# Kernel tuning notes

Hardware: AMD Instinct MI355X
Metric: run time of the kernel (lower is better)

Reference implementation:

```python
import jax, jax.numpy as jnp
import numpy as np

N_NODES = 200_000
N_EVENTS = 50_000
MEM = 128
RAW = 64
TD = 64
HEADS = 2
DH = MEM // HEADS
EDGE_DIM = RAW + TD
MSG_IN = 2 * MEM + RAW + TD


def _time_enc(x, w, b):
    # PyG TimeEncoder: cos(Linear(t)) with Linear(1, time_dim)
    return jnp.cos(x[..., None] * w + b)


def setup_inputs() -> dict:
    key = jax.random.key(0)
    ks = jax.random.split(key, 30)

    def w(i, shape, scale=None):
        s = scale if scale is not None else 1.0 / np.sqrt(shape[-1])
        return jax.random.normal(ks[i], shape, jnp.float32) * s

    src = jax.random.randint(ks[0], (N_EVENTS,), 0, N_NODES)
    dst = jax.random.randint(ks[1], (N_EVENTS,), 0, N_NODES)
    t = jnp.sort(jax.random.uniform(ks[2], (N_EVENTS,), jnp.float32, 0.0, 1e4))
    return dict(
        memory=w(3, (N_NODES, MEM), 1.0),
        last_update=jnp.zeros((N_NODES,), jnp.float32),
        t=t,
        msg=w(4, (N_EVENTS, RAW), 1.0),
        src=src, dst=dst,
        time_w=w(5, (TD,), 1.0), time_b=w(6, (TD,), 1.0),
        gru_Wih=w(7, (3 * MEM, MSG_IN)), gru_bih=w(8, (3 * MEM,), 0.02),
        gru_Whh=w(9, (3 * MEM, MEM)), gru_bhh=w(10, (3 * MEM,), 0.02),
        Wq=w(11, (MEM, MEM)), bq=w(12, (MEM,), 0.02),
        Wk=w(13, (MEM, MEM)), bk=w(14, (MEM,), 0.02),
        Wv=w(15, (MEM, MEM)), bv=w(16, (MEM,), 0.02),
        We=w(17, (MEM, EDGE_DIM)),
        Wskip=w(18, (MEM, MEM)), bskip=w(19, (MEM,), 0.02),
        Wls=w(20, (MEM, MEM)), bls=w(21, (MEM,), 0.02),
        Wld=w(22, (MEM, MEM)), bld=w(23, (MEM,), 0.02),
        Wlf=w(24, (1, MEM)), blf=w(25, (1,), 0.02),
    )


def reference(memory, last_update, t, msg, src, dst, time_w, time_b,
              gru_Wih, gru_bih, gru_Whh, gru_bhh,
              Wq, bq, Wk, bk, Wv, bv, We, Wskip, bskip,
              Wls, bls, Wld, bld, Wlf, blf):
    N, D = memory.shape
    E = src.shape[0]
    # --- 1. IdentityMessage: raw store for src side and dst side of each event ---
    dt_s = t - last_update[src]
    dt_d = t - last_update[dst]
    m_s = jnp.concatenate([memory[src], memory[dst], msg, _time_enc(dt_s, time_w, time_b)], -1)
    m_d = jnp.concatenate([memory[dst], memory[src], msg, _time_enc(dt_d, time_w, time_b)], -1)
    all_msg = jnp.concatenate([m_s, m_d], 0)        # [2E, MSG_IN]
    all_id = jnp.concatenate([src, dst], 0)         # [2E]
    all_t = jnp.concatenate([t, t], 0)              # [2E]
    # --- 2. LastAggregator: keep the latest message per target node ---
    pos = jnp.arange(2 * E, dtype=jnp.int32)
    last_pos = jnp.full((N,), -1, jnp.int32).at[all_id].max(pos)
    is_last = last_pos[all_id] == pos               # [2E], exactly one True per touched node
    # --- 3. GRUCell memory update (computed per message, scattered for the last one) ---
    h = memory[all_id]
    gi = all_msg @ gru_Wih.T + gru_bih
    gh = h @ gru_Whh.T + gru_bhh
    ir, iz, i_n = jnp.split(gi, 3, -1)
    hr, hz, h_n = jnp.split(gh, 3, -1)
    r = jax.nn.sigmoid(ir + hr)
    zg = jax.nn.sigmoid(iz + hz)
    n = jnp.tanh(i_n + r * h_n)
    h_new = (1.0 - zg) * n + zg * h
    memory_new = memory.at[all_id].add(jnp.where(is_last[:, None], h_new - h, 0.0))
    last_update_new = last_update.at[all_id].max(jnp.where(is_last, all_t, -jnp.inf))
    # --- 4. GraphAttentionEmbedding: TransformerConv(heads=2, edge_dim) in eval mode ---
    rel_t = last_update_new[src] - t
    edge_attr = jnp.concatenate([_time_enc(rel_t, time_w, time_b), msg], -1)  # [E, EDGE_DIM]
    e_proj = edge_attr @ We.T                                                  # [E, MEM]
    q = (memory_new @ Wq.T + bq).reshape(N, HEADS, DH)
    k = (memory_new[src] @ Wk.T + bk + e_proj).reshape(E, HEADS, DH)
    v = (memory_new[src] @ Wv.T + bv + e_proj).reshape(E, HEADS, DH)
    logit = jnp.einsum('ehd,ehd->eh', q[dst], k) / np.sqrt(DH).astype(np.float32)
    mx = jnp.full((N, HEADS), -jnp.inf, memory.dtype).at[dst].max(logit)
    a = jnp.exp(logit - mx[dst])
    denom = jax.ops.segment_sum(a, dst, num_segments=N)
    attn = a / denom[dst]                                                      # segment softmax over incoming edges
    out = jnp.zeros((N, HEADS, DH), memory.dtype).at[dst].add(attn[..., None] * v)
    z = out.reshape(N, D) + memory_new @ Wskip.T + bskip                       # root/skip connection
    # --- 5. LinkPredictor on event endpoints ---
    hlp = jax.nn.relu(z[src] @ Wls.T + bls + z[dst] @ Wld.T + bld)
    return hlp @ Wlf.T + blf                                                   # [E, 1]
```

## Files before the change

kernel.cpp:

```cpp
#include <hip/hip_runtime.h>
#include <math.h>

#define NN 200000
#define NE 50000
#define D 128

#define WGRU_SZ  196608
#define WATTN_SZ 147456
#define WSKP_SZ  16384
#define WLINK_SZ 32768

__device__ __forceinline__ float frcp_(float x) { return __builtin_amdgcn_rcpf(x); }
__device__ __forceinline__ float fsig_(float x) { return frcp_(1.f + __expf(-x)); }
__device__ __forceinline__ float ftanh_(float x) {
    float xc = fminf(fmaxf(x, -15.f), 15.f);
    float t = __expf(2.f * xc);
    return (t - 1.f) * frcp_(t + 1.f);
}

__device__ __forceinline__ unsigned short f2bf(float f) {
    unsigned int u = __float_as_uint(f);
    u = (u + 0x7fffu + ((u >> 16) & 1u)) >> 16;
    return (unsigned short)u;
}
__device__ __forceinline__ float bf2f(unsigned short b) {
    return __uint_as_float(((unsigned int)b) << 16);
}

typedef short bf16x8 __attribute__((ext_vector_type(8)));
typedef float f32x4  __attribute__((ext_vector_type(4)));

__global__ void k_initprep(const float* __restrict__ Wih, const float* __restrict__ Whh,
                           const float* __restrict__ Wk, const float* __restrict__ Wv,
                           const float* __restrict__ Wq, const float* __restrict__ We,
                           const float* __restrict__ Wskip,
                           const float* __restrict__ Wls, const float* __restrict__ Wld,
                           const int* __restrict__ src, const int* __restrict__ dst,
                           unsigned short* __restrict__ wgru,
                           unsigned short* __restrict__ wattn,
                           unsigned short* __restrict__ wskp,
                           unsigned short* __restrict__ wlink,
                           int* __restrict__ last_pos, int* __restrict__ count) {
    int idx = blockIdx.x * 256 + threadIdx.x;
    if (idx == 0) *count = 0;
    if (idx < 2 * NE) {
        int id = (idx < NE) ? src[idx] : dst[idx - NE];
        atomicMax(&last_pos[id], idx + 1);
    }
    if (idx >= 49152 + 36864 + 4096 + 8192) return;
    float4 v;
    unsigned short* dstp;
    int ncopies, stride;
    if (idx < 49152) {
        int n = idx / 96;
        int c = (idx - n * 96) * 4;
        if (n < 384) {
            v = *(const float4*)&Wih[n * 384 + c];
            if (n < 256 && c < 128) {
                const float4 w2 = *(const float4*)&Whh[n * 128 + c];
                v.x += w2.x; v.y += w2.y; v.z += w2.z; v.w += w2.w;
            }
        } else {
            if (c >= 128) return;
            v = *(const float4*)&Whh[(n - 128) * 128 + c];
        }
        dstp = &wgru[n * 384 + c]; ncopies = 8; stride = WGRU_SZ;
    } else if (idx < 49152 + 36864) {
        int i2 = idx - 49152;
        int n = i2 / 96;
        int c = (i2 - n * 96) * 4;
        if (n < 256) {
            const float* Wm = (n < 128) ? Wk : Wv;
            int nn = n & 127;
            if (c < 128)       v = *(const float4*)&Wm[nn * 128 + c];
            else if (c < 256)  v = *(const float4*)&We[nn * 128 + (c - 128)];
            else return;
        } else {
            if (c < 256) return;
            v = *(const float4*)&Wq[(n - 256) * 128 + (c - 256)];
        }
        dstp = &wattn[n * 384 + c]; ncopies = 4; stride = WATTN_SZ;
    } else if (idx < 49152 + 36864 + 4096) {
        int i3 = idx - 49152 - 36864;
        int n = i3 / 32;
        int c = (i3 - n * 32) * 4;
        v = *(const float4*)&Wskip[n * 128 + c];
        dstp = &wskp[n * 128 + c]; ncopies = 8; stride = WSKP_SZ;
    } else {
        int i4 = idx - 49152 - 36864 - 4096;
        int n = i4 / 64;
        int c = (i4 - n * 64) * 4;
        if (c < 128) v = *(const float4*)&Wls[n * 128 + c];
        else         v = *(const float4*)&Wld[n * 128 + (c - 128)];
        dstp = &wlink[n * 256 + c]; ncopies = 4; stride = WLINK_SZ;
    }
    ushort4 b;
    b.x = f2bf(v.x); b.y = f2bf(v.y); b.z = f2bf(v.z); b.w = f2bf(v.w);
    for (int r = 0; r < ncopies; ++r)
        *(ushort4*)(dstp + (size_t)r * stride) = b;
}

__global__ void k_compact(const int* __restrict__ src, const int* __restrict__ dst,
                          const int* __restrict__ last_pos,
                          int* __restrict__ count, int* __restrict__ clist,
                          int* __restrict__ node2slot, int* __restrict__ head) {
    int i = blockIdx.x * blockDim.x + threadIdx.x;
    if (i < 2 * NE) {
        int id = (i < NE) ? src[i] : dst[i - NE];
        if (last_pos[id] == i + 1) {
            int s = atomicAdd(count, 1);
            clist[s] = i;
            node2slot[id] = s;
            head[s] = -1;
        }
    }
}

#define GMB 64
__global__ __launch_bounds__(512) void k_gru(
    const float* __restrict__ memp, const float* __restrict__ lup,
    const float* __restrict__ tp, const float* __restrict__ msgp,
    const int* __restrict__ srcp, const int* __restrict__ dstp,
    const float* __restrict__ twp, const float* __restrict__ tbp,
    const int* __restrict__ clist,
    const unsigned short* __restrict__ wgru_all,
    const float* __restrict__ bih, const float* __restrict__ bhh,
    const unsigned short* __restrict__ wskp_all, const float* __restrict__ bskip,
    const int* __restrict__ countp,
    unsigned short* __restrict__ mem_new, unsigned short* __restrict__ zbf,
    float* __restrict__ lu_new)
{
    __shared__ alignas(16) unsigned short Xs[64][392];
    __shared__ int sid[64], sother[64], se[64];
    __shared__ float sdt[64];
    int cnt = *countp;
    int base = blockIdx.x * GMB;
    if (base >= cnt) return;
    int tid = threadIdx.x;
    const unsigned short* __restrict__ wgru = wgru_all + (size_t)(blockIdx.x & 7) * WGRU_SZ;
    const unsigned short* __restrict__ wskp = wskp_all + (size_t)(blockIdx.x & 7) * WSKP_SZ;

    if (tid < 64) {
        int ii = base + tid;
        bool valid = ii < cnt;
        int iw = clist[valid ? ii : (cnt - 1)];
        int e = (iw < NE) ? iw : (iw - NE);
        int id    = (iw < NE) ? srcp[e] : dstp[e];
        int oth   = (iw < NE) ? dstp[e] : srcp[e];
        sid[tid] = id; sother[tid] = oth; se[tid] = e;
        float tt = tp[e];
        float lu = lup[id];
        sdt[tid] = tt - lu;
        if (valid) lu_new[id] = fmaxf(lu, tt);
    }
    __syncthreads();
    {
        int m = tid >> 3, li = tid & 7;
        int id = sid[m], oth = sother[m], e = se[m];
        float dt = sdt[m];
        #pragma unroll
        for (int j = 0; j < 12; ++j) {
            int c4 = li + 8 * j;
            float4 v;
            if (c4 < 32)      v = *(const float4*)&memp[id * D + c4 * 4];
            else if (c4 < 64) v = *(const float4*)&memp[oth * D + (c4 - 32) * 4];
            else if (c4 < 80) v = *(const float4*)&msgp[e * 64 + (c4 - 64) * 4];
            else {
                int c0 = (c4 - 80) * 4;
                v.x = cosf(dt * twp[c0 + 0] + tbp[c0 + 0]);
                v.y = cosf(dt * twp[c0 + 1] + tbp[c0 + 1]);
                v.z = cosf(dt * twp[c0 + 2] + tbp[c0 + 2]);
                v.w = cosf(dt * twp[c0 + 3] + tbp[c0 + 3]);
            }
            ushort4 b;
            b.x = f2bf(v.x); b.y = f2bf(v.y); b.z = f2bf(v.z); b.w = f2bf(v.w);
            *(ushort4*)&Xs[m][c4 * 4] = b;
        }
    }
    __syncthreads();

    int lane = tid & 63, w = tid >> 6;
    int q = lane >> 4, l15 = lane & 15;
    int q8 = q * 8, w16 = w * 16;

    f32x4 acc[4][4];
    #pragma unroll
    for (int mt = 0; mt < 4; ++mt)
        #pragma unroll
        for (int g = 0; g < 4; ++g)
            acc[mt][g] = (f32x4)(0.0f);

#define GRU_STEP(NG)                                                                      \
    {                                                                                     \
        bf16x8 a[4];                                                                      \
        _Pragma("unroll")                                                                 \
        for (int mt = 0; mt < 4; ++mt) a[mt] = *(const bf16x8*)&Xs[mt * 16 + l15][k0 + q8]; \
        _Pragma("unroll")                                                                 \
        for (int g = 0; g < NG; ++g) {                                                    \
            const bf16x8 b = *(const bf16x8*)&wgru[(g * 128 + w16 + l15) * 384 + k0 + q8]; \
            _Pragma("unroll")                                                             \
            for (int mt = 0; mt < 4; ++mt)                                                \
                acc[mt][g] = __builtin_amdgcn_mfma_f32_16x16x32_bf16(a[mt], b, acc[mt][g], 0, 0, 0); \
        }                                                                                 \
    }

    #pragma unroll 2
    for (int ks = 0; ks < 4; ++ks) { int k0 = ks * 32; GRU_STEP(4) }
    #pragma unroll 2
    for (int ks = 4; ks < 12; ++ks) { int k0 = ks * 32; GRU_STEP(3) }
#undef GRU_STEP

    float nval[4][4];
    {
        int c = w16 + l15;
        float br  = bih[c]       + bhh[c];
        float bz  = bih[128 + c] + bhh[128 + c];
        float bin = bih[256 + c];
        float bhn = bhh[256 + c];
        #pragma unroll
        for (int mt = 0; mt < 4; ++mt) {
            #pragma unroll
            for (int reg = 0; reg < 4; ++reg) {
                int m = mt * 16 + q * 4 + reg;
                float r  = fsig_(acc[mt][0][reg] + br);
                float zg = fsig_(acc[mt][1][reg] + bz);
                float n  = ftanh_(acc[mt][2][reg] + bin + r * (acc[mt][3][reg] + bhn));
                float hv = bf2f(Xs[m][c]);
                nval[mt][reg] = (1.f - zg) * n + zg * hv;
            }
        }
    }

    __syncthreads();
    {
        int c = w16 + l15;
        #pragma unroll
        for (int mt = 0; mt < 4; ++mt)
            #pragma unroll
            for (int reg = 0; reg < 4; ++reg)
                Xs[mt * 16 + q * 4 + reg][c] = f2bf(nval[mt][reg]);
    }
    __syncthreads();

    {
        #pragma unroll
        for (int j = 0; j < 2; ++j) {
            int ch = tid + 512 * j;
            int m = ch >> 4, c8 = ch & 15;
            *(uint4*)&mem_new[(size_t)(base + m) * D + c8 * 8] = *(const uint4*)&Xs[m][c8 * 8];
        }
    }

    f32x4 acc2[4];
    #pragma unroll
    for (int mt = 0; mt < 4; ++mt) acc2[mt] = (f32x4)(0.0f);
    #pragma unroll
    for (int ks = 0; ks < 4; ++ks) {
        int k0 = ks * 32;
        bf16x8 a[4];
        #pragma unroll
        for (int mt = 0; mt < 4; ++mt) a[mt] = *(const bf16x8*)&Xs[mt * 16 + l15][k0 + q8];
        const bf16x8 b = *(const bf16x8*)&wskp[(w16 + l15) * 128 + k0 + q8];
        #pragma unroll
        for (int mt = 0; mt < 4; ++mt)
            acc2[mt] = __builtin_amdgcn_mfma_f32_16x16x32_bf16(a[mt], b, acc2[mt], 0, 0, 0);
    }
    __syncthreads();
    {
        int ch = w16 + l15;
        float b = bskip[ch];
        #pragma unroll
        for (int mt = 0; mt < 4; ++mt)
            #pragma unroll
            for (int reg = 0; reg < 4; ++reg)
                Xs[mt * 16 + q * 4 + reg][ch] = f2bf(acc2[mt][reg] + b);
    }
    __syncthreads();
    {
        #pragma unroll
        for (int j = 0; j < 2; ++j) {
            int ch = tid + 512 * j;
            int m = ch >> 4, c8 = ch & 15;
            *(uint4*)&zbf[(size_t)(base + m) * D + c8 * 8] = *(const uint4*)&Xs[m][c8 * 8];
        }
    }
}

#define AMB 32
__global__ __launch_bounds__(256) void k_attnA(
    const int* __restrict__ srcp, const int* __restrict__ dstp,
    const float* __restrict__ tp, const float* __restrict__ msgp,
    const float* __restrict__ twp, const float* __restrict__ tbp,
    const float* __restrict__ lu_new, const int* __restrict__ node2slot,
    const unsigned short* __restrict__ mem_new,
    const unsigned short* __restrict__ wattn_all,
    const float* __restrict__ bq, const float* __restrict__ bk, const float* __restrict__ bv,
    unsigned short* __restrict__ vbuf, float* __restrict__ abuf,
    int* __restrict__ head, int* __restrict__ next)
{
    __shared__ alignas(16) unsigned short Xs[32][392];
    unsigned short (*kLb)[136] = (unsigned short(*)[136])(&Xs[0][0]);
    unsigned short (*qLb)[136] = (unsigned short(*)[136])(&Xs[0][0] + 4352);
    __shared__ float sa[AMB][2];
    __shared__ int sslot[AMB], sdslot[AMB];
    __shared__ float srel[AMB];
    int tid = threadIdx.x;
    int e0 = blockIdx.x * AMB;
    const unsigned short* __restrict__ wattn = wattn_all + (size_t)(blockIdx.x & 3) * WATTN_SZ;
    {
        int gid = blockIdx.x * 256 + tid;
        if (gid < NE) {
            int sl = node2slot[dstp[gid]];
            next[gid] = atomicExch(&head[sl], gid);
        }
    }
    if (tid < AMB) {
        int e = e0 + tid; if (e >= NE) e = NE - 1;
        int s = srcp[e], dd = dstp[e];
        sslot[tid]  = node2slot[s];
        sdslot[tid] = node2slot[dd];
        srel[tid] = lu_new[s] - tp[e];
    }
    __syncthreads();
    {
        int m = tid >> 3, li = tid & 7;
        int e = e0 + m; if (e >= NE) e = NE - 1;
        int ssl = sslot[m], dsl = sdslot[m];
        float rel = srel[m];
        uint4* xrow = (uint4*)&Xs[m][0];
        const uint4* srow = (const uint4*)&mem_new[(size_t)ssl * D];
        const uint4* drow = (const uint4*)&mem_new[(size_t)dsl * D];
        #pragma unroll
        for (int j = 0; j < 2; ++j) {
            xrow[li + 8 * j]      = srow[li + 8 * j];
            xrow[32 + li + 8 * j] = drow[li + 8 * j];
        }
        {
            int c0 = li * 8;
            ushort4 lo, hi;
            lo.x = f2bf(cosf(rel * twp[c0 + 0] + tbp[c0 + 0]));
            lo.y = f2bf(cosf(rel * twp[c0 + 1] + tbp[c0 + 1]));
            lo.z = f2bf(cosf(rel * twp[c0 + 2] + tbp[c0 + 2]));
            lo.w = f2bf(cosf(rel * twp[c0 + 3] + tbp[c0 + 3]));
            hi.x = f2bf(cosf(rel * twp[c0 + 4] + tbp[c0 + 4]));
            hi.y = f2bf(cosf(rel * twp[c0 + 5] + tbp[c0 + 5]));
            hi.z = f2bf(cosf(rel * twp[c0 + 6] + tbp[c0 + 6]));
            hi.w = f2bf(cosf(rel * twp[c0 + 7] + tbp[c0 + 7]));
            *(ushort4*)&Xs[m][128 + c0]     = lo;
            *(ushort4*)&Xs[m][128 + c0 + 4] = hi;
        }
        {
            float4 a = *(const float4*)&msgp[e * 64 + li * 8];
            float4 b = *(const float4*)&msgp[e * 64 + li * 8 + 4];
            ushort4 lo, hi;
            lo.x = f2bf(a.x); lo.y = f2bf(a.y); lo.z = f2bf(a.z); lo.w = f2bf(a.w);
            hi.x = f2bf(b.x); hi.y = f2bf(b.y); hi.z = f2bf(b.z); hi.w = f2bf(b.w);
            *(ushort4*)&Xs[m][192 + li * 8]     = lo;
            *(ushort4*)&Xs[m][192 + li * 8 + 4] = hi;
        }
    }
    __syncthreads();

    int lane = tid & 63, w = tid >> 6;
    int q = lane >> 4, l15 = lane & 15;
    int q8 = q * 8;

    f32x4 acc[2][6];
    #pragma unroll
    for (int mt = 0; mt < 2; ++mt)
        #pragma unroll
        for (int jj = 0; jj < 6; ++jj) acc[mt][jj] = (f32x4)(0.0f);

    #pragma unroll 2
    for (int ks = 0; ks < 8; ++ks) {
        int k0 = ks * 32;
        const bf16x8 a0 = *(const bf16x8*)&Xs[l15][k0 + q8];
        const bf16x8 a1 = *(const bf16x8*)&Xs[16 + l15][k0 + q8];
        #pragma unroll
        for (int jj = 0; jj < 4; ++jj) {
            int nt = w + 4 * jj;
            const bf16x8 b = *(const bf16x8*)&wattn[(nt * 16 + l15) * 384 + k0 + q8];
            acc[0][jj] = __builtin_amdgcn_mfma_f32_16x16x32_bf16(a0, b, acc[0][jj], 0, 0, 0);
            acc[1][jj] = __builtin_amdgcn_mfma_f32_16x16x32_bf16(a1, b, acc[1][jj], 0, 0, 0);
        }
    }
    #pragma unroll 2
    for (int ks = 8; ks < 12; ++ks) {
        int k0 = ks * 32;
        const bf16x8 a0 = *(const bf16x8*)&Xs[l15][k0 + q8];
        const bf16x8 a1 = *(const bf16x8*)&Xs[16 + l15][k0 + q8];
        #pragma unroll
        for (int jj = 4; jj < 6; ++jj) {
            int nt = w + 4 * jj;
            const bf16x8 b = *(const bf16x8*)&wattn[(nt * 16 + l15) * 384 + k0 + q8];
            acc[0][jj] = __builtin_amdgcn_mfma_f32_16x16x32_bf16(a0, b, acc[0][jj], 0, 0, 0);
            acc[1][jj] = __builtin_amdgcn_mfma_f32_16x16x32_bf16(a1, b, acc[1][jj], 0, 0, 0);
        }
    }

    __syncthreads();

    float vreg[2][2][4];
    #pragma unroll
    for (int jj = 0; jj < 6; ++jj) {
        int nt = w + 4 * jj;
        int gate = nt >> 3;
        int ch = (nt & 7) * 16 + l15;
        float bias = (gate == 0) ? bk[ch] : (gate == 1) ? bv[ch] : bq[ch];
        #pragma unroll
        for (int mt = 0; mt < 2; ++mt)
            #pragma unroll
            for (int reg = 0; reg < 4; ++reg) {
                int m = mt * 16 + q * 4 + reg;
                float val = acc[mt][jj][reg] + bias;
                if (gate == 0)      kLb[m][ch] = f2bf(val);
                else if (gate == 2) qLb[m][ch] = f2bf(val);
                else                vreg[jj - 2][mt][reg] = val;
            }
    }
    __syncthreads();
    #pragma unroll
    for (int pr = 0; pr < 16; ++pr) {
        int p2 = pr * 4 + w;
        int m = p2 >> 1, h = p2 & 1;
        float prod = bf2f(qLb[m][h * 64 + lane]) * bf2f(kLb[m][h * 64 + lane]);
        #pragma unroll
        for (int off = 32; off; off >>= 1) prod += __shfl_down(prod, off);
        if (lane == 0) {
            float a = __expf(prod * 0.125f);
            sa[m][h] = a;
            if (e0 + m < NE) abuf[(e0 + m) * 2 + h] = a;
        }
    }
    __syncthreads();
    {
        unsigned short (*vL)[136] = qLb;
        #pragma unroll
        for (int jv = 0; jv < 2; ++jv) {
            int ch = w * 16 + jv * 64 + l15;
            int h = jv;
            #pragma unroll
            for (int mt = 0; mt < 2; ++mt)
                #pragma unroll
                for (int reg = 0; reg < 4; ++reg) {
                    int m = mt * 16 + q * 4 + reg;
                    vL[m][ch] = f2bf(sa[m][h] * vreg[jv][mt][reg]);
                }
        }
        __syncthreads();
        #pragma unroll
        for (int j = 0; j < 2; ++j) {
            int chunk = tid + 256 * j;
            int row = chunk >> 4, c8 = chunk & 15;
            if (e0 + row < NE)
                *(uint4*)&vbuf[(size_t)(e0 + row) * D + c8 * 8] = *(const uint4*)&vL[row][c8 * 8];
        }
    }
}

__global__ __launch_bounds__(256) void k_gather(
    const int* __restrict__ countp, const int* __restrict__ head,
    const int* __restrict__ next, const float* __restrict__ abuf,
    const unsigned short* __restrict__ vbuf, unsigned short* __restrict__ zbf)
{
    int cnt = *countp;
    int slot = blockIdx.x * 32 + (threadIdx.x >> 3);
    if (slot >= cnt) return;
    int li = threadIdx.x & 7;
    int c0 = li * 16;
    int h = li >> 2;
    float vsum[16];
    #pragma unroll
    for (int j = 0; j < 16; ++j) vsum[j] = 0.f;
    float asum = 0.f;
    for (int e = head[slot]; e != -1; e = next[e]) {
        asum += abuf[e * 2 + h];
        uint4 v0 = *(const uint4*)&vbuf[(size_t)e * D + c0];
        uint4 v1 = *(const uint4*)&vbuf[(size_t)e * D + c0 + 8];
        const unsigned short* pv0 = (const unsigned short*)&v0;
        const unsigned short* pv1 = (const unsigned short*)&v1;
        #pragma unroll
        for (int j = 0; j < 8; ++j) { vsum[j] += bf2f(pv0[j]); vsum[8 + j] += bf2f(pv1[j]); }
    }
    if (asum > 0.f) {
        float rr = frcp_(asum);
        uint4 z0 = *(const uint4*)&zbf[(size_t)slot * D + c0];
        uint4 z1 = *(const uint4*)&zbf[(size_t)slot * D + c0 + 8];
        const unsigned short* pz0 = (const unsigned short*)&z0;
        const unsigned short* pz1 = (const unsigned short*)&z1;
        unsigned short o[16];
        #pragma unroll
        for (int j = 0; j < 8; ++j) {
            o[j]     = f2bf(bf2f(pz0[j]) + vsum[j] * rr);
            o[8 + j] = f2bf(bf2f(pz1[j]) + vsum[8 + j] * rr);
        }
        *(uint4*)&zbf[(size_t)slot * D + c0]     = *(const uint4*)&o[0];
        *(uint4*)&zbf[(size_t)slot * D + c0 + 8] = *(const uint4*)&o[8];
    }
}

__global__ __launch_bounds__(256) void k_link(
    const int* __restrict__ srcp, const int* __restrict__ dstp,
    const int* __restrict__ node2slot,
    const unsigned short* __restrict__ zbf,
    const unsigned short* __restrict__ wlink_all,
    const float* __restrict__ bls, const float* __restrict__ bld,
    const float* __restrict__ Wlf, const float* __restrict__ blf,
    float* __restrict__ outp)
{
    __shared__ alignas(16) unsigned short Xs[32][264];
    __shared__ int ssl[32], sdl[32];
    __shared__ float sred[32][4];
    int tid = threadIdx.x;
    int e0 = blockIdx.x * 32;
    const unsigned short* __restrict__ wlink = wlink_all + (size_t)(blockIdx.x & 3) * WLINK_SZ;
    if (tid < 32) {
        int e = e0 + tid; if (e >= NE) e = NE - 1;
        ssl[tid] = node2slot[srcp[e]];
        sdl[tid] = node2slot[dstp[e]];
    }
    __syncthreads();
    {
        int m = tid >> 3, li = tid & 7;
        uint4* xrow = (uint4*)&Xs[m][0];
        const uint4* srow = (const uint4*)&zbf[(size_t)ssl[m] * D];
        const uint4* drow = (const uint4*)&zbf[(size_t)sdl[m] * D];
        xrow[li]      = srow[li];
        xrow[li + 8]  = srow[li + 8];
        xrow[16 + li] = drow[li];
        xrow[24 + li] = drow[li + 8];
    }
    __syncthreads();

    int lane = tid & 63, w = tid >> 6;
    int q = lane >> 4, l15 = lane & 15;
    int q8 = q * 8;

    f32x4 acc[2][2];
    #pragma unroll
    for (int mt = 0; mt < 2; ++mt)
        #pragma unroll
        for (int jj = 0; jj < 2; ++jj) acc[mt][jj] = (f32x4)(0.0f);

    #pragma unroll
    for (int ks = 0; ks < 8; ++ks) {
        int k0 = ks * 32;
        const bf16x8 a0 = *(const bf16x8*)&Xs[l15][k0 + q8];
        const bf16x8 a1 = *(const bf16x8*)&Xs[16 + l15][k0 + q8];
        #pragma unroll
        for (int jj = 0; jj < 2; ++jj) {
            int nt = w + 4 * jj;
            const bf16x8 b = *(const bf16x8*)&wlink[(nt * 16 + l15) * 256 + k0 + q8];
            acc[0][jj] = __builtin_amdgcn_mfma_f32_16x16x32_bf16(a0, b, acc[0][jj], 0, 0, 0);
            acc[1][jj] = __builtin_amdgcn_mfma_f32_16x16x32_bf16(a1, b, acc[1][jj], 0, 0, 0);
        }
    }

    float p[2][4];
    #pragma unroll
    for (int mt = 0; mt < 2; ++mt)
        #pragma unroll
        for (int reg = 0; reg < 4; ++reg) p[mt][reg] = 0.f;
    #pragma unroll
    for (int jj = 0; jj < 2; ++jj) {
        int ch = (w + 4 * jj) * 16 + l15;
        float bias = bls[ch] + bld[ch];
        float wl = Wlf[ch];
        #pragma unroll
        for (int mt = 0; mt < 2; ++mt)
            #pragma unroll
            for (int reg = 0; reg < 4; ++reg)
                p[mt][reg] += fmaxf(acc[mt][jj][reg] + bias, 0.f) * wl;
    }
    #pragma unroll
    for (int mask = 1; mask < 16; mask <<= 1) {
        #pragma unroll
        for (int mt = 0; mt < 2; ++mt)
            #pragma unroll
            for (int reg = 0; reg < 4; ++reg)
                p[mt][reg] += __shfl_xor(p[mt][reg], mask);
    }
    if (l15 == 0) {
        #pragma unroll
        for (int mt = 0; mt < 2; ++mt)
            #pragma unroll
            for (int reg = 0; reg < 4; ++reg)
                sred[mt * 16 + q * 4 + reg][w] = p[mt][reg];
    }
    __syncthreads();
    if (tid < 32) {
        int e = e0 + tid;
        if (e < NE)
            outp[e] = sred[tid][0] + sred[tid][1] + sred[tid][2] + sred[tid][3] + blf[0];
    }
}

extern "C" void kernel_launch(void* const* d_in, const int* in_sizes, int n_in,
                              void* d_out, int out_size, void* d_ws, size_t ws_size,
                              hipStream_t stream)
{
    const float* memory      = (const float*)d_in[0];
    const float* last_update = (const float*)d_in[1];
    const float* t           = (const float*)d_in[2];
    const float* msg         = (const float*)d_in[3];
    const int*   src         = (const int*)d_in[4];
    const int*   dst         = (const int*)d_in[5];
    const float* time_w      = (const float*)d_in[6];
    const float* time_b      = (const float*)d_in[7];
    const float* gru_Wih     = (const float*)d_in[8];
    const float* gru_bih     = (const float*)d_in[9];
    const float* gru_Whh     = (const float*)d_in[10];
    const float* gru_bhh     = (const float*)d_in[11];
    const float* Wq          = (const float*)d_in[12];
    const float* bq          = (const float*)d_in[13];
    const float* Wk          = (const float*)d_in[14];
    const float* bk          = (const float*)d_in[15];
    const float* Wv          = (const float*)d_in[16];
    const float* bv          = (const float*)d_in[17];
    const float* We          = (const float*)d_in[18];
    const float* Wskip       = (const float*)d_in[19];
    const float* bskip       = (const float*)d_in[20];
    const float* Wls         = (const float*)d_in[21];
    const float* bls         = (const float*)d_in[22];
    const float* Wld         = (const float*)d_in[23];
    const float* bld         = (const float*)d_in[24];
    const float* Wlf         = (const float*)d_in[25];
    const float* blf         = (const float*)d_in[26];
    float* outp = (float*)d_out;

    char* ws = (char*)d_ws;
    int*   last_pos  = (int*)  (ws + 0);
    int*   node2slot = (int*)  (ws + 800000);
    float* lu_new    = (float*)(ws + 1600000);
    int*   count     = (int*)  (ws + 2400000);
    int*   clist     = (int*)  (ws + 2400016);
    unsigned short* wgru    = (unsigned short*)(ws + 79624592);
    unsigned short* wattn   = (unsigned short*)(ws + 82770320);
    unsigned short* wskp    = (unsigned short*)(ws + 83949968);
    unsigned short* wlink   = (unsigned short*)(ws + 84212112);
    unsigned short* mem_new = (unsigned short*)(ws + 84474256);
    unsigned short* zbf     = (unsigned short*)(ws + 110082448);
    unsigned short* vbuf    = (unsigned short*)(ws + 135690640);
    float* abuf = (float*)(ws + 148490640);
    int*   head = (int*)  (ws + 148890640);
    int*   next = (int*)  (ws + 149290768);

    k_initprep<<<(2 * NE + 255) / 256, 256, 0, stream>>>(
                 gru_Wih, gru_Whh, Wk, Wv, Wq, We, Wskip, Wls, Wld, src, dst,
                 wgru, wattn, wskp, wlink, last_pos, count);
    k_compact <<<(2 * NE + 255) / 256, 256, 0, stream>>>(src, dst, last_pos, count,
                 clist, node2slot, head);
    k_gru     <<<(2 * NE + GMB - 1) / GMB, 512, 0, stream>>>(memory, last_update, t, msg,
                 src, dst, time_w, time_b, clist, wgru, gru_bih, gru_bhh,
                 wskp, bskip, count, mem_new, zbf, lu_new);
    k_attnA   <<<(NE + AMB - 1) / AMB, 256, 0, stream>>>(src, dst, t, msg, time_w, time_b,
                 lu_new, node2slot, mem_new, wattn, bq, bk, bv, vbuf, abuf, head, next);
    k_gather  <<<(2 * NE + 31) / 32, 256, 0, stream>>>(count, head, next, abuf, vbuf, zbf);
    k_link    <<<(NE + 31) / 32, 256, 0, stream>>>(src, dst, node2slot, zbf,
                 wlink, bls, bld, Wlf, blf, outp);
}
```

Measured before the change: 385.3 us.

## Fold skip projection into link predictor weights via concatenated z rows

Removes the per-node skip GEMM from the GRU kernel by precomputing Wls·Wskip and Wld·Wskip (and the folded biases) at init. The GRU writes memory_new into the upper half of a 256-wide zcat row, and the gather kernel writes the attention output into the lower half. The link kernel then does a single K=512 GEMM over both halves, with 64 events per block. This trades a smaller GRU kernel and one fewer round trip through global memory for a larger link GEMM, a serial 128-length dot-product loop per thread at init, and an occupancy hint on k_gru.

Result: slower. 400.9 us (+4.0%).

```diff
diff --git a/kernel.cpp b/kernel.cpp
--- a/kernel.cpp
+++ b/kernel.cpp
@@ -4,11 +4,11 @@
 #define NN 200000
 #define NE 50000
 #define D 128
+#define ZROW 256
 
 #define WGRU_SZ  196608
 #define WATTN_SZ 147456
-#define WSKP_SZ  16384
-#define WLINK_SZ 32768
+#define WLNK2_SZ 65536
 
 __device__ __forceinline__ float frcp_(float x) { return __builtin_amdgcn_rcpf(x); }
 __device__ __forceinline__ float fsig_(float x) { return frcp_(1.f + __expf(-x)); }
@@ -33,13 +33,14 @@
 __global__ void k_initprep(const float* __restrict__ Wih, const float* __restrict__ Whh,
                            const float* __restrict__ Wk, const float* __restrict__ Wv,
                            const float* __restrict__ Wq, const float* __restrict__ We,
-                           const float* __restrict__ Wskip,
+                           const float* __restrict__ Wskip, const float* __restrict__ bskip,
                            const float* __restrict__ Wls, const float* __restrict__ Wld,
+                           const float* __restrict__ bls, const float* __restrict__ bld,
                            const int* __restrict__ src, const int* __restrict__ dst,
                            unsigned short* __restrict__ wgru,
                            unsigned short* __restrict__ wattn,
-                           unsigned short* __restrict__ wskp,
-                           unsigned short* __restrict__ wlink,
+                           unsigned short* __restrict__ wlink2,
+                           float* __restrict__ blink,
                            int* __restrict__ last_pos, int* __restrict__ count) {
     int idx = blockIdx.x * 256 + threadIdx.x;
     if (idx == 0) *count = 0;
@@ -47,7 +48,7 @@
         int id = (idx < NE) ? src[idx] : dst[idx - NE];
         atomicMax(&last_pos[id], idx + 1);
     }
-    if (idx >= 49152 + 36864 + 4096 + 8192) return;
+    if (idx >= 102528) return;
     float4 v;
     unsigned short* dstp;
     int ncopies, stride;
@@ -80,19 +81,39 @@
             v = *(const float4*)&Wq[(n - 256) * 128 + (c - 256)];
         }
         dstp = &wattn[n * 384 + c]; ncopies = 4; stride = WATTN_SZ;
-    } else if (idx < 49152 + 36864 + 4096) {
-        int i3 = idx - 49152 - 36864;
-        int n = i3 / 32;
-        int c = (i3 - n * 32) * 4;
-        v = *(const float4*)&Wskip[n * 128 + c];
-        dstp = &wskp[n * 128 + c]; ncopies = 8; stride = WSKP_SZ;
+    } else if (idx < 86016 + 8192) {
+        int i4 = idx - 86016;
+        int n = i4 >> 6;
+        int c = (i4 & 63) * 4;
+        int dc;
+        if (c < 128) { v = *(const float4*)&Wls[n * 128 + c];        dc = c; }
+        else         { v = *(const float4*)&Wld[n * 128 + (c - 128)]; dc = c + 128; }
+        dstp = &wlink2[n * 512 + dc]; ncopies = 4; stride = WLNK2_SZ;
+    } else if (idx < 94208 + 8192) {
+        int i5 = idx - 94208;
+        int n = i5 >> 6;
+        int g = i5 & 63;
+        const float* Wrow = (g < 32) ? &Wls[n * 128] : &Wld[n * 128];
+        int c = (g & 31) * 4;
+        float ax = 0.f, ay = 0.f, az = 0.f, aw = 0.f;
+        for (int j = 0; j < 128; ++j) {
+            float a = Wrow[j];
+            const float4 ws = *(const float4*)&Wskip[j * 128 + c];
+            ax += a * ws.x; ay += a * ws.y; az += a * ws.z; aw += a * ws.w;
+        }
+        ushort4 b4;
+        b4.x = f2bf(ax); b4.y = f2bf(ay); b4.z = f2bf(az); b4.w = f2bf(aw);
+        unsigned short* dp = &wlink2[n * 512 + ((g < 32) ? 128 : 384) + c];
+        for (int r = 0; r < 4; ++r)
+            *(ushort4*)(dp + (size_t)r * WLNK2_SZ) = b4;
+        return;
     } else {
-        int i4 = idx - 49152 - 36864 - 4096;
-        int n = i4 / 64;
-        int c = (i4 - n * 64) * 4;
-        if (c < 128) v = *(const float4*)&Wls[n * 128 + c];
-        else         v = *(const float4*)&Wld[n * 128 + (c - 128)];
-        dstp = &wlink[n * 256 + c]; ncopies = 4; stride = WLINK_SZ;
+        int n = idx - 102400;
+        float s = bls[n] + bld[n];
+        for (int j = 0; j < 128; ++j)
+            s += (Wls[n * 128 + j] + Wld[n * 128 + j]) * bskip[j];
+        blink[n] = s;
+        return;
     }
     ushort4 b;
     b.x = f2bf(v.x); b.y = f2bf(v.y); b.z = f2bf(v.z); b.w = f2bf(v.w);
@@ -117,7 +138,7 @@
 }
 
 #define GMB 64
-__global__ __launch_bounds__(512) void k_gru(
+__global__ __launch_bounds__(512, 4) void k_gru(
     const float* __restrict__ memp, const float* __restrict__ lup,
     const float* __restrict__ tp, const float* __restrict__ msgp,
     const int* __restrict__ srcp, const int* __restrict__ dstp,
@@ -125,9 +146,8 @@
     const int* __restrict__ clist,
     const unsigned short* __restrict__ wgru_all,
     const float* __restrict__ bih, const float* __restrict__ bhh,
-    const unsigned short* __restrict__ wskp_all, const float* __restrict__ bskip,
     const int* __restrict__ countp,
-    unsigned short* __restrict__ mem_new, unsigned short* __restrict__ zbf,
+    unsigned short* __restrict__ zcat,
     float* __restrict__ lu_new)
 {
     __shared__ alignas(16) unsigned short Xs[64][392];
@@ -138,7 +158,6 @@
     if (base >= cnt) return;
     int tid = threadIdx.x;
     const unsigned short* __restrict__ wgru = wgru_all + (size_t)(blockIdx.x & 7) * WGRU_SZ;
-    const unsigned short* __restrict__ wskp = wskp_all + (size_t)(blockIdx.x & 7) * WSKP_SZ;
 
     if (tid < 64) {
         int ii = base + tid;
@@ -247,41 +266,8 @@
         for (int j = 0; j < 2; ++j) {
             int ch = tid + 512 * j;
             int m = ch >> 4, c8 = ch & 15;
-            *(uint4*)&mem_new[(size_t)(base + m) * D + c8 * 8] = *(const uint4*)&Xs[m][c8 * 8];
-        }
-    }
-
-    f32x4 acc2[4];
-    #pragma unroll
-    for (int mt = 0; mt < 4; ++mt) acc2[mt] = (f32x4)(0.0f);
-    #pragma unroll
-    for (int ks = 0; ks < 4; ++ks) {
-        int k0 = ks * 32;
-        bf16x8 a[4];
-        #pragma unroll
-        for (int mt = 0; mt < 4; ++mt) a[mt] = *(const bf16x8*)&Xs[mt * 16 + l15][k0 + q8];
-        const bf16x8 b = *(const bf16x8*)&wskp[(w16 + l15) * 128 + k0 + q8];
-        #pragma unroll
-        for (int mt = 0; mt < 4; ++mt)
-            acc2[mt] = __builtin_amdgcn_mfma_f32_16x16x32_bf16(a[mt], b, acc2[mt], 0, 0, 0);
-    }
-    __syncthreads();
-    {
-        int ch = w16 + l15;
-        float b = bskip[ch];
-        #pragma unroll
-        for (int mt = 0; mt < 4; ++mt)
-            #pragma unroll
-            for (int reg = 0; reg < 4; ++reg)
-                Xs[mt * 16 + q * 4 + reg][ch] = f2bf(acc2[mt][reg] + b);
-    }
-    __syncthreads();
-    {
-        #pragma unroll
-        for (int j = 0; j < 2; ++j) {
-            int ch = tid + 512 * j;
-            int m = ch >> 4, c8 = ch & 15;
-            *(uint4*)&zbf[(size_t)(base + m) * D + c8 * 8] = *(const uint4*)&Xs[m][c8 * 8];
+            *(uint4*)&zcat[(size_t)(base + m) * ZROW + 128 + c8 * 8] =
+                *(const uint4*)&Xs[m][c8 * 8];
         }
     }
 }
@@ -292,7 +278,7 @@
     const float* __restrict__ tp, const float* __restrict__ msgp,
     const float* __restrict__ twp, const float* __restrict__ tbp,
     const float* __restrict__ lu_new, const int* __restrict__ node2slot,
-    const unsigned short* __restrict__ mem_new,
+    const unsigned short* __restrict__ zcat,
     const unsigned short* __restrict__ wattn_all,
     const float* __restrict__ bq, const float* __restrict__ bk, const float* __restrict__ bv,
     unsigned short* __restrict__ vbuf, float* __restrict__ abuf,
@@ -328,8 +314,8 @@
         int ssl = sslot[m], dsl = sdslot[m];
         float rel = srel[m];
         uint4* xrow = (uint4*)&Xs[m][0];
-        const uint4* srow = (const uint4*)&mem_new[(size_t)ssl * D];
-        const uint4* drow = (const uint4*)&mem_new[(size_t)dsl * D];
+        const uint4* srow = (const uint4*)&zcat[(size_t)ssl * ZROW + 128];
+        const uint4* drow = (const uint4*)&zcat[(size_t)dsl * ZROW + 128];
         #pragma unroll
         for (int j = 0; j < 2; ++j) {
             xrow[li + 8 * j]      = srow[li + 8 * j];
@@ -461,7 +447,7 @@
 __global__ __launch_bounds__(256) void k_gather(
     const int* __restrict__ countp, const int* __restrict__ head,
     const int* __restrict__ next, const float* __restrict__ abuf,
-    const unsigned short* __restrict__ vbuf, unsigned short* __restrict__ zbf)
+    const unsigned short* __restrict__ vbuf, unsigned short* __restrict__ zcat)
 {
     int cnt = *countp;
     int slot = blockIdx.x * 32 + (threadIdx.x >> 3);
@@ -482,53 +468,46 @@
         #pragma unroll
         for (int j = 0; j < 8; ++j) { vsum[j] += bf2f(pv0[j]); vsum[8 + j] += bf2f(pv1[j]); }
     }
-    if (asum > 0.f) {
-        float rr = frcp_(asum);
-        uint4 z0 = *(const uint4*)&zbf[(size_t)slot * D + c0];
-        uint4 z1 = *(const uint4*)&zbf[(size_t)slot * D + c0 + 8];
-        const unsigned short* pz0 = (const unsigned short*)&z0;
-        const unsigned short* pz1 = (const unsigned short*)&z1;
-        unsigned short o[16];
-        #pragma unroll
-        for (int j = 0; j < 8; ++j) {
-            o[j]     = f2bf(bf2f(pz0[j]) + vsum[j] * rr);
-            o[8 + j] = f2bf(bf2f(pz1[j]) + vsum[8 + j] * rr);
-        }
-        *(uint4*)&zbf[(size_t)slot * D + c0]     = *(const uint4*)&o[0];
-        *(uint4*)&zbf[(size_t)slot * D + c0 + 8] = *(const uint4*)&o[8];
-    }
-}
-
+    float rr = (asum > 0.f) ? frcp_(asum) : 0.f;
+    unsigned short o[16];
+    #pragma unroll
+    for (int j = 0; j < 16; ++j) o[j] = f2bf(vsum[j] * rr);
+    *(uint4*)&zcat[(size_t)slot * ZROW + c0]     = *(const uint4*)&o[0];
+    *(uint4*)&zcat[(size_t)slot * ZROW + c0 + 8] = *(const uint4*)&o[8];
+}
+
+#define ALB 64
 __global__ __launch_bounds__(256) void k_link(
     const int* __restrict__ srcp, const int* __restrict__ dstp,
     const int* __restrict__ node2slot,
-    const unsigned short* __restrict__ zbf,
-    const unsigned short* __restrict__ wlink_all,
-    const float* __restrict__ bls, const float* __restrict__ bld,
+    const unsigned short* __restrict__ zcat,
+    const unsigned short* __restrict__ wlink2_all,
+    const float* __restrict__ blink,
     const float* __restrict__ Wlf, const float* __restrict__ blf,
     float* __restrict__ outp)
 {
-    __shared__ alignas(16) unsigned short Xs[32][264];
-    __shared__ int ssl[32], sdl[32];
-    __shared__ float sred[32][4];
+    __shared__ alignas(16) unsigned short Xs[64][520];
+    __shared__ int ssl[64], sdl[64];
+    __shared__ float sred[64][4];
     int tid = threadIdx.x;
-    int e0 = blockIdx.x * 32;
-    const unsigned short* __restrict__ wlink = wlink_all + (size_t)(blockIdx.x & 3) * WLINK_SZ;
-    if (tid < 32) {
+    int e0 = blockIdx.x * ALB;
+    const unsigned short* __restrict__ wlink2 = wlink2_all + (size_t)(blockIdx.x & 3) * WLNK2_SZ;
+    if (tid < ALB) {
         int e = e0 + tid; if (e >= NE) e = NE - 1;
         ssl[tid] = node2slot[srcp[e]];
         sdl[tid] = node2slot[dstp[e]];
     }
     __syncthreads();
     {
-        int m = tid >> 3, li = tid & 7;
+        int m = tid >> 2, li = tid & 3;
         uint4* xrow = (uint4*)&Xs[m][0];
-        const uint4* srow = (const uint4*)&zbf[(size_t)ssl[m] * D];
-        const uint4* drow = (const uint4*)&zbf[(size_t)sdl[m] * D];
-        xrow[li]      = srow[li];
-        xrow[li + 8]  = srow[li + 8];
-        xrow[16 + li] = drow[li];
-        xrow[24 + li] = drow[li + 8];
+        const uint4* srow = (const uint4*)&zcat[(size_t)ssl[m] * ZROW];
+        const uint4* drow = (const uint4*)&zcat[(size_t)sdl[m] * ZROW];
+        #pragma unroll
+        for (int j = 0; j < 8; ++j) {
+            xrow[li + 4 * j]      = srow[li + 4 * j];
+            xrow[32 + li + 4 * j] = drow[li + 4 * j];
+        }
     }
     __syncthreads();
 
@@ -536,38 +515,40 @@
     int q = lane >> 4, l15 = lane & 15;
     int q8 = q * 8;
 
-    f32x4 acc[2][2];
-    #pragma unroll
-    for (int mt = 0; mt < 2; ++mt)
+    f32x4 acc[4][2];
+    #pragma unroll
+    for (int mt = 0; mt < 4; ++mt)
         #pragma unroll
         for (int jj = 0; jj < 2; ++jj) acc[mt][jj] = (f32x4)(0.0f);
 
-    #pragma unroll
-    for (int ks = 0; ks < 8; ++ks) {
+    #pragma unroll 2
+    for (int ks = 0; ks < 16; ++ks) {
         int k0 = ks * 32;
-        const bf16x8 a0 = *(const bf16x8*)&Xs[l15][k0 + q8];
-        const bf16x8 a1 = *(const bf16x8*)&Xs[16 + l15][k0 + q8];
+        bf16x8 a[4];
+        #pragma unroll
+        for (int mt = 0; mt < 4; ++mt) a[mt] = *(const bf16x8*)&Xs[mt * 16 + l15][k0 + q8];
         #pragma unroll
         for (int jj = 0; jj < 2; ++jj) {
             int nt = w + 4 * jj;
-            const bf16x8 b = *(const bf16x8*)&wlink[(nt * 16 + l15) * 256 + k0 + q8];
-            acc[0][jj] = __builtin_amdgcn_mfma_f32_16x16x32_bf16(a0, b, acc[0][jj], 0, 0, 0);
-            acc[1][jj] = __builtin_amdgcn_mfma_f32_16x16x32_bf16(a1, b, acc[1][jj], 0, 0, 0);
-        }
-    }
-
-    float p[2][4];
-    #pragma unroll
-    for (int mt = 0; mt < 2; ++mt)
+            const bf16x8 b = *(const bf16x8*)&wlink2[(nt * 16 + l15) * 512 + k0 + q8];
+            #pragma unroll
+            for (int mt = 0; mt < 4; ++mt)
+                acc[mt][jj] = __builtin_amdgcn_mfma_f32_16x16x32_bf16(a[mt], b, acc[mt][jj], 0, 0, 0);
+        }
+    }
+
+    float p[4][4];
+    #pragma unroll
+    for (int mt = 0; mt < 4; ++mt)
         #pragma unroll
         for (int reg = 0; reg < 4; ++reg) p[mt][reg] = 0.f;
     #pragma unroll
     for (int jj = 0; jj < 2; ++jj) {
         int ch = (w + 4 * jj) * 16 + l15;
-        float bias = bls[ch] + bld[ch];
+        float bias = blink[ch];
         float wl = Wlf[ch];
         #pragma unroll
-        for (int mt = 0; mt < 2; ++mt)
+        for (int mt = 0; mt < 4; ++mt)
             #pragma unroll
             for (int reg = 0; reg < 4; ++reg)
                 p[mt][reg] += fmaxf(acc[mt][jj][reg] + bias, 0.f) * wl;
@@ -575,20 +556,20 @@
     #pragma unroll
     for (int mask = 1; mask < 16; mask <<= 1) {
         #pragma unroll
-        for (int mt = 0; mt < 2; ++mt)
+        for (int mt = 0; mt < 4; ++mt)
             #pragma unroll
             for (int reg = 0; reg < 4; ++reg)
                 p[mt][reg] += __shfl_xor(p[mt][reg], mask);
     }
     if (l15 == 0) {
         #pragma unroll
-        for (int mt = 0; mt < 2; ++mt)
+        for (int mt = 0; mt < 4; ++mt)
             #pragma unroll
             for (int reg = 0; reg < 4; ++reg)
                 sred[mt * 16 + q * 4 + reg][w] = p[mt][reg];
     }
     __syncthreads();
-    if (tid < 32) {
+    if (tid < ALB) {
         int e = e0 + tid;
         if (e < NE)
             outp[e] = sred[tid][0] + sred[tid][1] + sred[tid][2] + sred[tid][3] + blf[0];
@@ -634,28 +615,27 @@
     float* lu_new    = (float*)(ws + 1600000);
     int*   count     = (int*)  (ws + 2400000);
     int*   clist     = (int*)  (ws + 2400016);
+    unsigned short* wlink2  = (unsigned short*)(ws + 2800016);
+    float* blink   = (float*)(ws + 3324304);
     unsigned short* wgru    = (unsigned short*)(ws + 79624592);
     unsigned short* wattn   = (unsigned short*)(ws + 82770320);
-    unsigned short* wskp    = (unsigned short*)(ws + 83949968);
-    unsigned short* wlink   = (unsigned short*)(ws + 84212112);
-    unsigned short* mem_new = (unsigned short*)(ws + 84474256);
-    unsigned short* zbf     = (unsigned short*)(ws + 110082448);
+    unsigned short* zcat    = (unsigned short*)(ws + 84474256);
     unsigned short* vbuf    = (unsigned short*)(ws + 135690640);
     float* abuf = (float*)(ws + 148490640);
     int*   head = (int*)  (ws + 148890640);
     int*   next = (int*)  (ws + 149290768);
 
-    k_initprep<<<(2 * NE + 255) / 256, 256, 0, stream>>>(
-                 gru_Wih, gru_Whh, Wk, Wv, Wq, We, Wskip, Wls, Wld, src, dst,
-                 wgru, wattn, wskp, wlink, last_pos, count);
+    k_initprep<<<401, 256, 0, stream>>>(
+                 gru_Wih, gru_Whh, Wk, Wv, Wq, We, Wskip, bskip, Wls, Wld, bls, bld,
+                 src, dst, wgru, wattn, wlink2, blink, last_pos, count);
     k_compact <<<(2 * NE + 255) / 256, 256, 0, stream>>>(src, dst, last_pos, count,
                  clist, node2slot, head);
     k_gru     <<<(2 * NE + GMB - 1) / GMB, 512, 0, stream>>>(memory, last_update, t, msg,
                  src, dst, time_w, time_b, clist, wgru, gru_bih, gru_bhh,
-                 wskp, bskip, count, mem_new, zbf, lu_new);
+                 count, zcat, lu_new);
     k_attnA   <<<(NE + AMB - 1) / AMB, 256, 0, stream>>>(src, dst, t, msg, time_w, time_b,
-                 lu_new, node2slot, mem_new, wattn, bq, bk, bv, vbuf, abuf, head, next);
-    k_gather  <<<(2 * NE + 31) / 32, 256, 0, stream>>>(count, head, next, abuf, vbuf, zbf);
-    k_link    <<<(NE + 31) / 32, 256, 0, stream>>>(src, dst, node2slot, zbf,
-                 wlink, bls, bld, Wlf, blf, outp);
-}
+                 lu_new, node2slot, zcat, wattn, bq, bk, bv, vbuf, abuf, head, next);
+    k_gather  <<<(2 * NE + 31) / 32, 256, 0, stream>>>(count, head, next, abuf, vbuf, zcat);
+    k_link    <<<(NE + ALB - 1) / ALB, 256, 0, stream>>>(src, dst, node2slot, zcat,
+                 wlink2, blink, Wlf, blf, outp);
+}
```
